# Kernel tuning notes

Hardware: AMD Instinct MI355X
Metric: run time of the kernel (lower is better)

Reference implementation:

```python
import jax, jax.numpy as jnp
import numpy as np
import math

N_COARSE, N_FINE = 8192, 32768
DEC_DIM, ENC_DIM, OUT_DIM, K = 256, 128, 128, 16
LN_EPS = 1e-5


def setup_inputs() -> dict:
    key = jax.random.key(0)
    ks = jax.random.split(key, 16)
    s = lambda fan_in: 1.0 / math.sqrt(fan_in)
    return {
        "decoder_features": jax.random.normal(ks[0], (N_COARSE, DEC_DIM), jnp.float32),
        "decoder_pos": jax.random.normal(ks[1], (N_COARSE, 3), jnp.float32),
        "encoder_features": jax.random.normal(ks[2], (N_FINE, ENC_DIM), jnp.float32),
        "encoder_pos": jax.random.normal(ks[3], (N_FINE, 3), jnp.float32),
        "encoder_labels": jax.random.randint(ks[4], (N_FINE,), 0, 13, jnp.int64),
        # params (torch nn.Linear default init scale)
        "Wq": jax.random.uniform(ks[5], (DEC_DIM, ENC_DIM), jnp.float32, -s(ENC_DIM), s(ENC_DIM)),
        "bq": jnp.zeros((DEC_DIM,), jnp.float32),
        "Wk": jax.random.uniform(ks[6], (DEC_DIM, DEC_DIM), jnp.float32, -s(DEC_DIM), s(DEC_DIM)),
        "bk": jnp.zeros((DEC_DIM,), jnp.float32),
        "Wv": jax.random.uniform(ks[7], (DEC_DIM, DEC_DIM), jnp.float32, -s(DEC_DIM), s(DEC_DIM)),
        "bv": jnp.zeros((DEC_DIM,), jnp.float32),
        "W1": jax.random.uniform(ks[8], (OUT_DIM, DEC_DIM + ENC_DIM), jnp.float32, -s(DEC_DIM + ENC_DIM), s(DEC_DIM + ENC_DIM)),
        "b1": jnp.zeros((OUT_DIM,), jnp.float32),
        "W2": jax.random.uniform(ks[9], (OUT_DIM, OUT_DIM), jnp.float32, -s(OUT_DIM), s(OUT_DIM)),
        "b2": jnp.zeros((OUT_DIM,), jnp.float32),
        "ln_g": jnp.ones((OUT_DIM,), jnp.float32),
        "ln_b": jnp.zeros((OUT_DIM,), jnp.float32),
    }


def _knn_indices(encoder_pos, decoder_pos, k):
    # For each fine (encoder) point, k nearest coarse (decoder) points.
    # squared distances [N_fine, N_coarse]
    d2 = (
        jnp.sum(encoder_pos * encoder_pos, axis=1, keepdims=True)
        - 2.0 * encoder_pos @ decoder_pos.T
        + jnp.sum(decoder_pos * decoder_pos, axis=1)[None, :]
    )
    _, idx = jax.lax.top_k(-d2, k)  # [N_fine, K]
    return idx


def reference(decoder_features, decoder_pos, encoder_features, encoder_pos,
              encoder_labels, Wq, bq, Wk, bk, Wv, bv, W1, b1, W2, b2, ln_g, ln_b):
    idx = _knn_indices(encoder_pos, decoder_pos, K)            # [Nf, K]
    nbr = decoder_features[idx]                                 # [Nf, K, Dd]
    query = encoder_features @ Wq.T + bq                        # [Nf, Dd]
    keys = nbr @ Wk.T + bk                                      # [Nf, K, Dd]
    values = nbr @ Wv.T + bv                                    # [Nf, K, Dd]
    scores = jnp.einsum('nd,nkd->nk', query, keys) / math.sqrt(DEC_DIM)
    # segment softmax over edges grouped by fine target == softmax over K
    weights = jax.nn.softmax(scores, axis=-1)                   # [Nf, K]
    agg = jnp.einsum('nk,nkd->nd', weights, values)             # [Nf, Dd]
    combined = jnp.concatenate([agg, encoder_features], axis=-1)
    h = jax.nn.relu(combined @ W1.T + b1)
    up = h @ W2.T + b2                                          # [Nf, out]
    mu = jnp.mean(up, axis=-1, keepdims=True)
    var = jnp.var(up, axis=-1, keepdims=True)
    out = (up - mu) * jax.lax.rsqrt(var + LN_EPS) * ln_g + ln_b
    # dropout is identity in eval mode
    return (out, encoder_pos, encoder_labels)
```

## Files before the change

kernel.cpp:

```cpp
#include <hip/hip_runtime.h>
#include <hip/hip_bf16.h>

typedef __hip_bfloat16 bf16;
typedef unsigned short u16;

#define NC 8192
#define NF 32768
#define DD 256
#define DE 128
#define KNN 16
#define FMAXV 3.402823466e+38f

__device__ __forceinline__ float bfbits2f(u16 u){
  union { unsigned u; float f; } x; x.u = ((unsigned)u) << 16; return x.f;
}

__global__ __launch_bounds__(256) void k_prep(const float* __restrict__ dpos,
                                              const float* __restrict__ Wk,
                                              const float* __restrict__ Wv,
                                              const float* __restrict__ W1,
                                              const float* __restrict__ W2,
                                              float4* __restrict__ pos4,
                                              float4* __restrict__ WkS,
                                              float4* __restrict__ WvS,
                                              float4* __restrict__ W1aS,
                                              float4* __restrict__ W1eSa,
                                              float4* __restrict__ W1eSb,
                                              float4* __restrict__ W2Sa,
                                              float4* __restrict__ W2Sb){
  int g = blockIdx.x * 256 + threadIdx.x;
  if (g < 8192){
    float x = dpos[g * 3 + 0], y = dpos[g * 3 + 1], z = dpos[g * 3 + 2];
    float dd = __fadd_rn(__fadd_rn(__fmul_rn(x,x), __fmul_rn(y,y)), __fmul_rn(z,z));
    pos4[g] = make_float4(x, y, z, dd * 0.5f);
  } else if (g < 24576){
    int f = g - 8192; int c4 = f >> 8, t = f & 255;
    WkS[f] = ((const float4*)(Wk + (size_t)t * 256))[c4];
  } else if (g < 40960){
    int f = g - 24576; int c4 = f >> 8, t = f & 255;
    WvS[f] = ((const float4*)(Wv + (size_t)t * 256))[c4];
  } else if (g < 49152){
    int f = g - 40960; int c4 = f >> 7, h = f & 127;
    W1aS[f] = ((const float4*)(W1 + (size_t)h * 384))[c4];
  } else if (g < 51200){
    int f = g - 49152; int c4 = f >> 6, jg = f & 63;
    W1eSa[f] = ((const float4*)(W1 + (size_t)(2 * jg) * 384 + 256))[c4];
  } else if (g < 53248){
    int f = g - 51200; int c4 = f >> 6, jg = f & 63;
    W1eSb[f] = ((const float4*)(W1 + (size_t)(2 * jg + 1) * 384 + 256))[c4];
  } else if (g < 55296){
    int f = g - 53248; int c4 = f >> 6, jg = f & 63;
    W2Sa[f] = ((const float4*)(W2 + (size_t)(2 * jg) * 128))[c4];
  } else if (g < 57344){
    int f = g - 55296; int c4 = f >> 6, jg = f & 63;
    W2Sb[f] = ((const float4*)(W2 + (size_t)(2 * jg + 1) * 128))[c4];
  }
}

__global__ __launch_bounds__(256) void k_dec(const float* __restrict__ df,
                                             const float* __restrict__ Wq, const float* __restrict__ bq,
                                             const float4* __restrict__ WkS, const float* __restrict__ bk,
                                             const float4* __restrict__ WvS, const float* __restrict__ bv,
                                             const float4* __restrict__ W1aS,
                                             bf16* __restrict__ Zd, bf16* __restrict__ Ud,
                                             float* __restrict__ bqK){
  __shared__ float bufA[16 * 256];
  __shared__ float bufB[16 * 256];
  int t = threadIdx.x;
  int g0 = blockIdx.x * 16;
  for (int r = 0; r < 16; ++r)
    bufA[r * 256 + t] = df[(size_t)(g0 + r) * 256 + t];
  __syncthreads();
  float accK[16], accV[16];
  #pragma unroll
  for (int p = 0; p < 16; ++p){ accK[p] = 0.f; accV[p] = 0.f; }
  const float4* A4 = (const float4*)bufA;
  for (int c4 = 0; c4 < 64; ++c4){
    float4 wk = WkS[c4 * 256 + t];
    float4 wv = WvS[c4 * 256 + t];
    #pragma unroll
    for (int p = 0; p < 16; ++p){
      float4 a = A4[p * 64 + c4];
      accK[p] += wk.x*a.x + wk.y*a.y + wk.z*a.z + wk.w*a.w;
      accV[p] += wv.x*a.x + wv.y*a.y + wv.z*a.z + wv.w*a.w;
    }
  }
  float bkj = bk[t];
  float bvj = bv[t];
  __syncthreads();
  #pragma unroll
  for (int p = 0; p < 16; ++p){
    bufA[p * 256 + t] = accK[p] + bkj;
    bufB[p * 256 + t] = accV[p] + bvj;
  }
  __syncthreads();
  if (t < 16){
    float s = 0.f;
    for (int j = 0; j < 256; ++j) s += bq[j] * bufA[t * 256 + j];
    bqK[g0 + t] = s;
  }
  {
    int c = t & 127, pg = t >> 7;
    float acc[8];
    #pragma unroll
    for (int pp = 0; pp < 8; ++pp) acc[pp] = 0.f;
    for (int j0 = 0; j0 < 256; j0 += 8){
      float w[8];
      #pragma unroll
      for (int jj = 0; jj < 8; ++jj)
        w[jj] = Wq[(size_t)(j0 + jj) * 128 + c];
      #pragma unroll
      for (int pp = 0; pp < 8; ++pp){
        float4 a = ((const float4*)bufA)[(pg * 8 + pp) * 64 + (j0 >> 2)];
        float4 b = ((const float4*)bufA)[(pg * 8 + pp) * 64 + (j0 >> 2) + 1];
        acc[pp] += w[0]*a.x + w[1]*a.y + w[2]*a.z + w[3]*a.w
                 + w[4]*b.x + w[5]*b.y + w[6]*b.z + w[7]*b.w;
      }
    }
    #pragma unroll
    for (int pp = 0; pp < 8; ++pp)
      Zd[(size_t)(g0 + pg * 8 + pp) * 128 + c] = __float2bfloat16(acc[pp]);
  }
  {
    int h = t & 127, pg = t >> 7;
    float acc[8];
    #pragma unroll
    for (int pp = 0; pp < 8; ++pp) acc[pp] = 0.f;
    for (int c4 = 0; c4 < 64; ++c4){
      float4 w = W1aS[c4 * 128 + h];
      #pragma unroll
      for (int pp = 0; pp < 8; ++pp){
        float4 a = ((const float4*)bufB)[(pg * 8 + pp) * 64 + c4];
        acc[pp] += w.x*a.x + w.y*a.y + w.z*a.z + w.w*a.w;
      }
    }
    #pragma unroll
    for (int pp = 0; pp < 8; ++pp)
      Ud[(size_t)(g0 + pg * 8 + pp) * 128 + h] = __float2bfloat16(acc[pp]);
  }
}

__global__ __launch_bounds__(256) void k_attn(const float* __restrict__ epos,
                                              const float4* __restrict__ pos4,
                                              const float* __restrict__ ef,
                                              const bf16* __restrict__ Zd,
                                              const bf16* __restrict__ Ud,
                                              const float* __restrict__ bqK,
                                              bf16* __restrict__ hagg){
  __shared__ float smin[4 * 64];
  __shared__ float tauLDS[4];
  __shared__ int   cnt[4];
  __shared__ float lval[4][64];
  __shared__ int   lidx[4][64];

  int t = threadIdx.x, lane = t & 63, w = t >> 6;
  int n0 = blockIdx.x * 4;
  float ex[4], ey[4], ez[4];
  #pragma unroll
  for (int p = 0; p < 4; ++p){
    ex[p] = epos[(n0 + p) * 3 + 0];
    ey[p] = epos[(n0 + p) * 3 + 1];
    ez[p] = epos[(n0 + p) * 3 + 2];
  }
  const float4* base = pos4 + w * 2048;

  float vmin[4] = {FMAXV, FMAXV, FMAXV, FMAXV};
  #pragma unroll 4
  for (int s = 0; s < 32; ++s){
    float4 P = base[s * 64 + lane];
    #pragma unroll
    for (int p = 0; p < 4; ++p){
      float ed = fmaf(ez[p], P.z, fmaf(ey[p], P.y, ex[p] * P.x));
      vmin[p] = fminf(vmin[p], P.w - ed);
    }
  }
  #pragma unroll
  for (int k = 2; k <= 64; k <<= 1){
    #pragma unroll
    for (int j = k >> 1; j > 0; j >>= 1){
      bool keepmin = ((lane & j) == 0) == ((lane & k) == 0);
      #pragma unroll
      for (int p = 0; p < 4; ++p){
        float pv = __shfl_xor(vmin[p], j);
        vmin[p] = keepmin ? fminf(vmin[p], pv) : fmaxf(vmin[p], pv);
      }
    }
  }
  if (lane < 16){
    #pragma unroll
    for (int p = 0; p < 4; ++p) smin[p * 64 + w * 16 + lane] = vmin[p];
  }
  if (t < 4) cnt[t] = 0;
  __syncthreads();
  {
    float v = smin[w * 64 + lane];
    #pragma unroll
    for (int k = 2; k <= 64; k <<= 1){
      #pragma unroll
      for (int j = k >> 1; j > 0; j >>= 1){
        float pv = __shfl_xor(v, j);
        bool keepmin = ((lane & j) == 0) == ((lane & k) == 0);
        v = keepmin ? fminf(v, pv) : fmaxf(v, pv);
      }
    }
    if (lane == 16) tauLDS[w] = v;
  }
  __syncthreads();
  float tau0[4];
  #pragma unroll
  for (int p = 0; p < 4; ++p) tau0[p] = tauLDS[p];

  #pragma unroll 2
  for (int s = 0; s < 32; ++s){
    float4 P = base[s * 64 + lane];
    int cand = w * 2048 + s * 64 + lane;
    #pragma unroll
    for (int p = 0; p < 4; ++p){
      float ed = fmaf(ez[p], P.z, fmaf(ey[p], P.y, ex[p] * P.x));
      float val = P.w - ed;
      if (val <= tau0[p]){
        int slot = atomicAdd(&cnt[p], 1);
        if (slot < 64){ lval[p][slot] = val; lidx[p][slot] = cand; }
      }
    }
  }
  __syncthreads();

  int n = n0 + w;
  int c = cnt[w]; if (c > 64) c = 64;
  float v  = (lane < c) ? lval[w][lane] : FMAXV;
  int   id = (lane < c) ? lidx[w][lane] : 0x7fffffff;
  #pragma unroll
  for (int k = 2; k <= 64; k <<= 1){
    #pragma unroll
    for (int j = k >> 1; j > 0; j >>= 1){
      float pv  = __shfl_xor(v, j);
      int   pid = __shfl_xor(id, j);
      bool keepmin = ((lane & j) == 0) == ((lane & k) == 0);
      bool pless = (pv < v) || (pv == v && pid < id);
      bool take = keepmin ? pless : !pless;
      if (take){ v = pv; id = pid; }
    }
  }
  int topi = id;

  float2 eu = *(const float2*)(ef + (size_t)n * 128 + lane * 2);
  float sc = -FMAXV;
  #pragma unroll
  for (int k = 0; k < KNN; ++k){
    int ik = __shfl(topi, k);
    ushort2 zu = *(const ushort2*)((const u16*)Zd + (size_t)ik * 128 + lane * 2);
    float p = eu.x * bfbits2f(zu.x) + eu.y * bfbits2f(zu.y);
    #pragma unroll
    for (int off = 32; off >= 1; off >>= 1) p += __shfl_xor(p, off);
    float bz = bqK[ik];
    if (lane == k) sc = (p + bz) * (1.0f / 16.0f);
  }
  float mx = sc;
  #pragma unroll
  for (int off = 8; off >= 1; off >>= 1) mx = fmaxf(mx, __shfl_xor(mx, off));
  float e = (lane < KNN) ? __expf(sc - mx) : 0.f;
  float l = e;
  #pragma unroll
  for (int off = 8; off >= 1; off >>= 1) l += __shfl_xor(l, off);
  float wgt = (lane < KNN) ? (e / l) : 0.f;

  float a0 = 0.f, a1 = 0.f;
  #pragma unroll
  for (int k = 0; k < KNN; ++k){
    int ik = __shfl(topi, k);
    float wk = __shfl(wgt, k);
    ushort2 uu = *(const ushort2*)((const u16*)Ud + (size_t)ik * 128 + lane * 2);
    a0 = fmaf(wk, bfbits2f(uu.x), a0);
    a1 = fmaf(wk, bfbits2f(uu.y), a1);
  }
  bf16* hr = hagg + (size_t)n * 128 + lane * 2;
  hr[0] = __float2bfloat16(a0);
  hr[1] = __float2bfloat16(a1);
}

__global__ __launch_bounds__(256) void k_mlp(const bf16* __restrict__ hagg, const float* __restrict__ ef,
                                             const float4* __restrict__ W1eSa, const float4* __restrict__ W1eSb,
                                             const float* __restrict__ b1,
                                             const float4* __restrict__ W2Sa, const float4* __restrict__ W2Sb,
                                             const float* __restrict__ b2,
                                             const float* __restrict__ lng, const float* __restrict__ lnb,
                                             const float* __restrict__ epos, const int* __restrict__ lab,
                                             float* __restrict__ out){
  __shared__ float efs[16 * 128];
  __shared__ float hgs[16 * 128];
  __shared__ float hbuf[16 * 128];
  __shared__ float ubuf[16 * 128];
  __shared__ float stats[32];
  int t = threadIdx.x;
  int n0 = blockIdx.x * 16;
  {
    int gid = blockIdx.x * 256 + t;
    if (gid < NF){
      float* op = out + (size_t)NF * 128;
      op[gid * 3 + 0] = epos[gid * 3 + 0];
      op[gid * 3 + 1] = epos[gid * 3 + 1];
      op[gid * 3 + 2] = epos[gid * 3 + 2];
      out[(size_t)NF * 128 + (size_t)NF * 3 + gid] = (float)lab[gid];
    }
  }
  for (int f = t; f < 2048; f += 256){
    int r = f >> 7, c = f & 127;
    efs[f] = ef[(size_t)(n0 + r) * 128 + c];
    hgs[f] = __bfloat162float(hagg[(size_t)(n0 + r) * 128 + c]);
  }
  __syncthreads();
  int jg = t & 63, pg = t >> 6;
  int j0 = jg * 2, p0 = pg * 4;
  float acc[2][4];
  #pragma unroll
  for (int a = 0; a < 2; ++a)
    #pragma unroll
    for (int p = 0; p < 4; ++p) acc[a][p] = 0.f;
  const float4* efs4 = (const float4*)efs;
  for (int c4 = 0; c4 < 32; ++c4){
    float4 wa = W1eSa[c4 * 64 + jg], wb = W1eSb[c4 * 64 + jg];
    #pragma unroll
    for (int p = 0; p < 4; ++p){
      float4 x = efs4[(p0 + p) * 32 + c4];
      acc[0][p] += wa.x*x.x + wa.y*x.y + wa.z*x.z + wa.w*x.w;
      acc[1][p] += wb.x*x.x + wb.y*x.y + wb.z*x.z + wb.w*x.w;
    }
  }
  float b1a = b1[j0], b1b = b1[j0 + 1];
  #pragma unroll
  for (int p = 0; p < 4; ++p){
    hbuf[(p0 + p) * 128 + j0]     = fmaxf(acc[0][p] + b1a + hgs[(p0 + p) * 128 + j0],     0.f);
    hbuf[(p0 + p) * 128 + j0 + 1] = fmaxf(acc[1][p] + b1b + hgs[(p0 + p) * 128 + j0 + 1], 0.f);
  }
  __syncthreads();
  float acc2[2][4];
  #pragma unroll
  for (int a = 0; a < 2; ++a)
    #pragma unroll
    for (int p = 0; p < 4; ++p) acc2[a][p] = 0.f;
  const float4* hb4 = (const float4*)hbuf;
  for (int c4 = 0; c4 < 32; ++c4){
    float4 wa = W2Sa[c4 * 64 + jg], wb = W2Sb[c4 * 64 + jg];
    #pragma unroll
    for (int p = 0; p < 4; ++p){
      float4 x = hb4[(p0 + p) * 32 + c4];
      acc2[0][p] += wa.x*x.x + wa.y*x.y + wa.z*x.z + wa.w*x.w;
      acc2[1][p] += wb.x*x.x + wb.y*x.y + wb.z*x.z + wb.w*x.w;
    }
  }
  float b2a = b2[j0], b2b = b2[j0 + 1];
  float u[2][4];
  #pragma unroll
  for (int p = 0; p < 4; ++p){
    u[0][p] = acc2[0][p] + b2a;
    u[1][p] = acc2[1][p] + b2b;
    ubuf[(p0 + p) * 128 + j0]     = u[0][p];
    ubuf[(p0 + p) * 128 + j0 + 1] = u[1][p];
  }
  __syncthreads();
  {
    int p = t >> 4, qi = t & 15;
    const float* ub = &ubuf[p * 128 + qi * 8];
    float s = 0.f, s2 = 0.f;
    #pragma unroll
    for (int e2i = 0; e2i < 8; ++e2i){ float v = ub[e2i]; s += v; s2 += v * v; }
    #pragma unroll
    for (int off = 1; off < 16; off <<= 1){ s += __shfl_xor(s, off); s2 += __shfl_xor(s2, off); }
    if (qi == 0){
      float mu = s * (1.f / 128.f);
      float var = s2 * (1.f / 128.f) - mu * mu;
      stats[p] = mu;
      stats[16 + p] = rsqrtf(fmaxf(var, 0.f) + 1e-5f);
    }
  }
  __syncthreads();
  float ga = lng[j0], gb = lng[j0 + 1];
  float ba = lnb[j0], bbv = lnb[j0 + 1];
  #pragma unroll
  for (int p = 0; p < 4; ++p){
    float mu = stats[p0 + p], rs = stats[16 + p0 + p];
    out[(size_t)(n0 + p0 + p) * 128 + j0]     = (u[0][p] - mu) * rs * ga + ba;
    out[(size_t)(n0 + p0 + p) * 128 + j0 + 1] = (u[1][p] - mu) * rs * gb + bbv;
  }
}

extern "C" void kernel_launch(void* const* d_in, const int* in_sizes, int n_in,
                              void* d_out, int out_size, void* d_ws, size_t ws_size,
                              hipStream_t stream){
  const float* df   = (const float*)d_in[0];
  const float* dpos = (const float*)d_in[1];
  const float* ef   = (const float*)d_in[2];
  const float* epos = (const float*)d_in[3];
  const int*   lab  = (const int*)d_in[4];
  const float* Wq = (const float*)d_in[5];
  const float* bq = (const float*)d_in[6];
  const float* Wk = (const float*)d_in[7];
  const float* bk = (const float*)d_in[8];
  const float* Wv = (const float*)d_in[9];
  const float* bv = (const float*)d_in[10];
  const float* W1 = (const float*)d_in[11];
  const float* b1 = (const float*)d_in[12];
  const float* W2 = (const float*)d_in[13];
  const float* b2 = (const float*)d_in[14];
  const float* lng = (const float*)d_in[15];
  const float* lnb = (const float*)d_in[16];
  float* out = (float*)d_out;

  char* wsb = (char*)d_ws;
  float4* pos4  = (float4*)(wsb);
  bf16*   Zd    = (bf16*)(wsb + 131072);
  bf16*   Ud    = (bf16*)(wsb + 2228224);
  float*  bqK   = (float*)(wsb + 4325376);
  bf16*   hagg  = (bf16*)(wsb + 4358144);
  float4* WkS   = (float4*)(wsb + 12746752);
  float4* WvS   = (float4*)(wsb + 13008896);
  float4* W1aS  = (float4*)(wsb + 13271040);
  float4* W1eSa = (float4*)(wsb + 13402112);
  float4* W1eSb = (float4*)(wsb + 13434880);
  float4* W2Sa  = (float4*)(wsb + 13467648);
  float4* W2Sb  = (float4*)(wsb + 13500416);

  k_prep <<<224, 256, 0, stream>>>(dpos, Wk, Wv, W1, W2, pos4, WkS, WvS, W1aS, W1eSa, W1eSb, W2Sa, W2Sb);
  k_dec  <<<NC / 16, 256, 0, stream>>>(df, Wq, bq, WkS, bk, WvS, bv, W1aS, Zd, Ud, bqK);
  k_attn <<<NF / 4, 256, 0, stream>>>(epos, pos4, ef, Zd, Ud, bqK, hagg);
  k_mlp  <<<NF / 16, 256, 0, stream>>>(hagg, ef, W1eSa, W1eSb, b1, W2Sa, W2Sb, b2, lng, lnb, epos, lab, out);
  (void)in_sizes; (void)n_in; (void)out_size; (void)ws_size;
}
```

Before: 374.0 us.

## Split decoder and MLP kernels to drop shared-memory staging and raise occupancy

Splits the decoder projection kernel into two launches (K/V projection to global memory, then Q- and W1-folding projections), and splits the MLP kernel into a first-layer kernel and a second-layer-plus-LayerNorm kernel. Operands are now read directly from global memory (uniform per wave) instead of being staged in LDS, which removes large shared buffers and barriers and should let more blocks run concurrently. Wq is pre-transposed into a float4 layout in the prep kernel, and the kNN distance is folded into a single FMA chain. The cost is two extra launches and fp32 round-trips of K/V and the hidden activations through global memory.

```diff
diff --git a/kernel.cpp b/kernel.cpp
--- a/kernel.cpp
+++ b/kernel.cpp
@@ -6,8 +6,6 @@
 
 #define NC 8192
 #define NF 32768
-#define DD 256
-#define DE 128
 #define KNN 16
 #define FMAXV 3.402823466e+38f
 
@@ -20,10 +18,12 @@
                                               const float* __restrict__ Wv,
                                               const float* __restrict__ W1,
                                               const float* __restrict__ W2,
+                                              const float* __restrict__ Wq,
                                               float4* __restrict__ pos4,
                                               float4* __restrict__ WkS,
                                               float4* __restrict__ WvS,
                                               float4* __restrict__ W1aS,
+                                              float4* __restrict__ WqS,
                                               float4* __restrict__ W1eSa,
                                               float4* __restrict__ W1eSb,
                                               float4* __restrict__ W2Sa,
@@ -54,89 +54,74 @@
   } else if (g < 57344){
     int f = g - 55296; int c4 = f >> 6, jg = f & 63;
     W2Sb[f] = ((const float4*)(W2 + (size_t)(2 * jg + 1) * 128))[c4];
-  }
-}
-
-__global__ __launch_bounds__(256) void k_dec(const float* __restrict__ df,
-                                             const float* __restrict__ Wq, const float* __restrict__ bq,
-                                             const float4* __restrict__ WkS, const float* __restrict__ bk,
-                                             const float4* __restrict__ WvS, const float* __restrict__ bv,
-                                             const float4* __restrict__ W1aS,
-                                             bf16* __restrict__ Zd, bf16* __restrict__ Ud,
-                                             float* __restrict__ bqK){
-  __shared__ float bufA[16 * 256];
-  __shared__ float bufB[16 * 256];
+  } else if (g < 65536){
+    int f = g - 57344; int j4 = f >> 7, c = f & 127;
+    WqS[f] = make_float4(Wq[(size_t)(j4 * 4 + 0) * 128 + c],
+                         Wq[(size_t)(j4 * 4 + 1) * 128 + c],
+                         Wq[(size_t)(j4 * 4 + 2) * 128 + c],
+                         Wq[(size_t)(j4 * 4 + 3) * 128 + c]);
+  }
+}
+
+__global__ __launch_bounds__(256) void k_dec1(const float* __restrict__ df,
+                                              const float4* __restrict__ WkS, const float* __restrict__ bk,
+                                              const float4* __restrict__ WvS, const float* __restrict__ bv,
+                                              float* __restrict__ Kg, float* __restrict__ Vg){
   int t = threadIdx.x;
   int g0 = blockIdx.x * 16;
-  for (int r = 0; r < 16; ++r)
-    bufA[r * 256 + t] = df[(size_t)(g0 + r) * 256 + t];
-  __syncthreads();
   float accK[16], accV[16];
   #pragma unroll
   for (int p = 0; p < 16; ++p){ accK[p] = 0.f; accV[p] = 0.f; }
-  const float4* A4 = (const float4*)bufA;
   for (int c4 = 0; c4 < 64; ++c4){
     float4 wk = WkS[c4 * 256 + t];
     float4 wv = WvS[c4 * 256 + t];
     #pragma unroll
     for (int p = 0; p < 16; ++p){
-      float4 a = A4[p * 64 + c4];
+      float4 a = ((const float4*)(df + (size_t)(g0 + p) * 256))[c4];
       accK[p] += wk.x*a.x + wk.y*a.y + wk.z*a.z + wk.w*a.w;
       accV[p] += wv.x*a.x + wv.y*a.y + wv.z*a.z + wv.w*a.w;
     }
   }
-  float bkj = bk[t];
-  float bvj = bv[t];
-  __syncthreads();
+  float bkj = bk[t], bvj = bv[t];
   #pragma unroll
   for (int p = 0; p < 16; ++p){
-    bufA[p * 256 + t] = accK[p] + bkj;
-    bufB[p * 256 + t] = accV[p] + bvj;
-  }
-  __syncthreads();
+    Kg[(size_t)(g0 + p) * 256 + t] = accK[p] + bkj;
+    Vg[(size_t)(g0 + p) * 256 + t] = accV[p] + bvj;
+  }
+}
+
+__global__ __launch_bounds__(256) void k_dec2(const float* __restrict__ Kg,
+                                              const float* __restrict__ Vg,
+                                              const float4* __restrict__ WqS,
+                                              const float4* __restrict__ W1aS,
+                                              const float* __restrict__ bq,
+                                              bf16* __restrict__ Zd, bf16* __restrict__ Ud,
+                                              float* __restrict__ bqK){
+  int t = threadIdx.x;
+  int g0 = blockIdx.x * 16;
+  int half = __builtin_amdgcn_readfirstlane(t >> 7);
+  int c = t & 127;
+  const float*  src = half ? Vg : Kg;
+  const float4* W   = half ? W1aS : WqS;
+  float acc[16];
+  #pragma unroll
+  for (int p = 0; p < 16; ++p) acc[p] = 0.f;
+  for (int j4 = 0; j4 < 64; ++j4){
+    float4 w = W[j4 * 128 + c];
+    #pragma unroll
+    for (int p = 0; p < 16; ++p){
+      float4 a = ((const float4*)(src + (size_t)(g0 + p) * 256))[j4];
+      acc[p] += w.x*a.x + w.y*a.y + w.z*a.z + w.w*a.w;
+    }
+  }
+  bf16* dst = half ? Ud : Zd;
+  #pragma unroll
+  for (int p = 0; p < 16; ++p)
+    dst[(size_t)(g0 + p) * 128 + c] = __float2bfloat16(acc[p]);
   if (t < 16){
     float s = 0.f;
-    for (int j = 0; j < 256; ++j) s += bq[j] * bufA[t * 256 + j];
+    for (int j = 0; j < 256; ++j) s += bq[j] * Kg[(size_t)(g0 + t) * 256 + j];
     bqK[g0 + t] = s;
-  }
-  {
-    int c = t & 127, pg = t >> 7;
-    float acc[8];
-    #pragma unroll
-    for (int pp = 0; pp < 8; ++pp) acc[pp] = 0.f;
-    for (int j0 = 0; j0 < 256; j0 += 8){
-      float w[8];
-      #pragma unroll
-      for (int jj = 0; jj < 8; ++jj)
-        w[jj] = Wq[(size_t)(j0 + jj) * 128 + c];
-      #pragma unroll
-      for (int pp = 0; pp < 8; ++pp){
-        float4 a = ((const float4*)bufA)[(pg * 8 + pp) * 64 + (j0 >> 2)];
-        float4 b = ((const float4*)bufA)[(pg * 8 + pp) * 64 + (j0 >> 2) + 1];
-        acc[pp] += w[0]*a.x + w[1]*a.y + w[2]*a.z + w[3]*a.w
-                 + w[4]*b.x + w[5]*b.y + w[6]*b.z + w[7]*b.w;
-      }
-    }
-    #pragma unroll
-    for (int pp = 0; pp < 8; ++pp)
-      Zd[(size_t)(g0 + pg * 8 + pp) * 128 + c] = __float2bfloat16(acc[pp]);
-  }
-  {
-    int h = t & 127, pg = t >> 7;
-    float acc[8];
-    #pragma unroll
-    for (int pp = 0; pp < 8; ++pp) acc[pp] = 0.f;
-    for (int c4 = 0; c4 < 64; ++c4){
-      float4 w = W1aS[c4 * 128 + h];
-      #pragma unroll
-      for (int pp = 0; pp < 8; ++pp){
-        float4 a = ((const float4*)bufB)[(pg * 8 + pp) * 64 + c4];
-        acc[pp] += w.x*a.x + w.y*a.y + w.z*a.z + w.w*a.w;
-      }
-    }
-    #pragma unroll
-    for (int pp = 0; pp < 8; ++pp)
-      Ud[(size_t)(g0 + pg * 8 + pp) * 128 + h] = __float2bfloat16(acc[pp]);
   }
 }
 
@@ -155,12 +140,12 @@
 
   int t = threadIdx.x, lane = t & 63, w = t >> 6;
   int n0 = blockIdx.x * 4;
-  float ex[4], ey[4], ez[4];
+  float nex[4], ney[4], nez[4];
   #pragma unroll
   for (int p = 0; p < 4; ++p){
-    ex[p] = epos[(n0 + p) * 3 + 0];
-    ey[p] = epos[(n0 + p) * 3 + 1];
-    ez[p] = epos[(n0 + p) * 3 + 2];
+    nex[p] = -epos[(n0 + p) * 3 + 0];
+    ney[p] = -epos[(n0 + p) * 3 + 1];
+    nez[p] = -epos[(n0 + p) * 3 + 2];
   }
   const float4* base = pos4 + w * 2048;
 
@@ -170,8 +155,8 @@
     float4 P = base[s * 64 + lane];
     #pragma unroll
     for (int p = 0; p < 4; ++p){
-      float ed = fmaf(ez[p], P.z, fmaf(ey[p], P.y, ex[p] * P.x));
-      vmin[p] = fminf(vmin[p], P.w - ed);
+      float val = fmaf(nez[p], P.z, fmaf(ney[p], P.y, fmaf(nex[p], P.x, P.w)));
+      vmin[p] = fminf(vmin[p], val);
     }
   }
   #pragma unroll
@@ -216,8 +201,7 @@
     int cand = w * 2048 + s * 64 + lane;
     #pragma unroll
     for (int p = 0; p < 4; ++p){
-      float ed = fmaf(ez[p], P.z, fmaf(ey[p], P.y, ex[p] * P.x));
-      float val = P.w - ed;
+      float val = fmaf(nez[p], P.z, fmaf(ney[p], P.y, fmaf(nex[p], P.x, P.w)));
       if (val <= tau0[p]){
         int slot = atomicAdd(&cnt[p], 1);
         if (slot < 64){ lval[p][slot] = val; lidx[p][slot] = cand; }
@@ -279,17 +263,50 @@
   hr[1] = __float2bfloat16(a1);
 }
 
-__global__ __launch_bounds__(256) void k_mlp(const bf16* __restrict__ hagg, const float* __restrict__ ef,
-                                             const float4* __restrict__ W1eSa, const float4* __restrict__ W1eSb,
-                                             const float* __restrict__ b1,
-                                             const float4* __restrict__ W2Sa, const float4* __restrict__ W2Sb,
-                                             const float* __restrict__ b2,
-                                             const float* __restrict__ lng, const float* __restrict__ lnb,
-                                             const float* __restrict__ epos, const int* __restrict__ lab,
-                                             float* __restrict__ out){
-  __shared__ float efs[16 * 128];
-  __shared__ float hgs[16 * 128];
-  __shared__ float hbuf[16 * 128];
+__global__ __launch_bounds__(256) void k_mlp1(const bf16* __restrict__ hagg,
+                                              const float* __restrict__ ef,
+                                              const float4* __restrict__ W1eSa,
+                                              const float4* __restrict__ W1eSb,
+                                              const float* __restrict__ b1,
+                                              float* __restrict__ hg){
+  int t = threadIdx.x;
+  int jg = t & 63;
+  int pg4 = __builtin_amdgcn_readfirstlane((t >> 6) * 4);
+  int n0 = blockIdx.x * 16;
+  int j0 = jg * 2;
+  float acc[2][4];
+  #pragma unroll
+  for (int a = 0; a < 2; ++a)
+    #pragma unroll
+    for (int p = 0; p < 4; ++p) acc[a][p] = 0.f;
+  for (int c4 = 0; c4 < 32; ++c4){
+    float4 wa = W1eSa[c4 * 64 + jg];
+    float4 wb = W1eSb[c4 * 64 + jg];
+    #pragma unroll
+    for (int p = 0; p < 4; ++p){
+      float4 x = ((const float4*)(ef + (size_t)(n0 + pg4 + p) * 128))[c4];
+      acc[0][p] += wa.x*x.x + wa.y*x.y + wa.z*x.z + wa.w*x.w;
+      acc[1][p] += wb.x*x.x + wb.y*x.y + wb.z*x.z + wb.w*x.w;
+    }
+  }
+  float b1a = b1[j0], b1b = b1[j0 + 1];
+  #pragma unroll
+  for (int p = 0; p < 4; ++p){
+    size_t row = (size_t)(n0 + pg4 + p);
+    ushort2 hgv = *(const ushort2*)((const u16*)hagg + row * 128 + j0);
+    float h0 = fmaxf(acc[0][p] + b1a + bfbits2f(hgv.x), 0.f);
+    float h1 = fmaxf(acc[1][p] + b1b + bfbits2f(hgv.y), 0.f);
+    *(float2*)(hg + row * 128 + j0) = make_float2(h0, h1);
+  }
+}
+
+__global__ __launch_bounds__(256) void k_mlp2(const float* __restrict__ hg,
+                                              const float4* __restrict__ W2Sa,
+                                              const float4* __restrict__ W2Sb,
+                                              const float* __restrict__ b2,
+                                              const float* __restrict__ lng, const float* __restrict__ lnb,
+                                              const float* __restrict__ epos, const int* __restrict__ lab,
+                                              float* __restrict__ out){
   __shared__ float ubuf[16 * 128];
   __shared__ float stats[32];
   int t = threadIdx.x;
@@ -304,47 +321,20 @@
       out[(size_t)NF * 128 + (size_t)NF * 3 + gid] = (float)lab[gid];
     }
   }
-  for (int f = t; f < 2048; f += 256){
-    int r = f >> 7, c = f & 127;
-    efs[f] = ef[(size_t)(n0 + r) * 128 + c];
-    hgs[f] = __bfloat162float(hagg[(size_t)(n0 + r) * 128 + c]);
-  }
-  __syncthreads();
-  int jg = t & 63, pg = t >> 6;
-  int j0 = jg * 2, p0 = pg * 4;
-  float acc[2][4];
+  int jg = t & 63;
+  int pg4 = __builtin_amdgcn_readfirstlane((t >> 6) * 4);
+  int j0 = jg * 2;
+  float acc2[2][4];
   #pragma unroll
   for (int a = 0; a < 2; ++a)
     #pragma unroll
-    for (int p = 0; p < 4; ++p) acc[a][p] = 0.f;
-  const float4* efs4 = (const float4*)efs;
+    for (int p = 0; p < 4; ++p) acc2[a][p] = 0.f;
   for (int c4 = 0; c4 < 32; ++c4){
-    float4 wa = W1eSa[c4 * 64 + jg], wb = W1eSb[c4 * 64 + jg];
+    float4 wa = W2Sa[c4 * 64 + jg];
+    float4 wb = W2Sb[c4 * 64 + jg];
     #pragma unroll
     for (int p = 0; p < 4; ++p){
-      float4 x = efs4[(p0 + p) * 32 + c4];
-      acc[0][p] += wa.x*x.x + wa.y*x.y + wa.z*x.z + wa.w*x.w;
-      acc[1][p] += wb.x*x.x + wb.y*x.y + wb.z*x.z + wb.w*x.w;
-    }
-  }
-  float b1a = b1[j0], b1b = b1[j0 + 1];
-  #pragma unroll
-  for (int p = 0; p < 4; ++p){
-    hbuf[(p0 + p) * 128 + j0]     = fmaxf(acc[0][p] + b1a + hgs[(p0 + p) * 128 + j0],     0.f);
-    hbuf[(p0 + p) * 128 + j0 + 1] = fmaxf(acc[1][p] + b1b + hgs[(p0 + p) * 128 + j0 + 1], 0.f);
-  }
-  __syncthreads();
-  float acc2[2][4];
-  #pragma unroll
-  for (int a = 0; a < 2; ++a)
-    #pragma unroll
-    for (int p = 0; p < 4; ++p) acc2[a][p] = 0.f;
-  const float4* hb4 = (const float4*)hbuf;
-  for (int c4 = 0; c4 < 32; ++c4){
-    float4 wa = W2Sa[c4 * 64 + jg], wb = W2Sb[c4 * 64 + jg];
-    #pragma unroll
-    for (int p = 0; p < 4; ++p){
-      float4 x = hb4[(p0 + p) * 32 + c4];
+      float4 x = ((const float4*)(hg + (size_t)(n0 + pg4 + p) * 128))[c4];
       acc2[0][p] += wa.x*x.x + wa.y*x.y + wa.z*x.z + wa.w*x.w;
       acc2[1][p] += wb.x*x.x + wb.y*x.y + wb.z*x.z + wb.w*x.w;
     }
@@ -355,8 +345,8 @@
   for (int p = 0; p < 4; ++p){
     u[0][p] = acc2[0][p] + b2a;
     u[1][p] = acc2[1][p] + b2b;
-    ubuf[(p0 + p) * 128 + j0]     = u[0][p];
-    ubuf[(p0 + p) * 128 + j0 + 1] = u[1][p];
+    ubuf[(pg4 + p) * 128 + j0]     = u[0][p];
+    ubuf[(pg4 + p) * 128 + j0 + 1] = u[1][p];
   }
   __syncthreads();
   {
@@ -379,9 +369,9 @@
   float ba = lnb[j0], bbv = lnb[j0 + 1];
   #pragma unroll
   for (int p = 0; p < 4; ++p){
-    float mu = stats[p0 + p], rs = stats[16 + p0 + p];
-    out[(size_t)(n0 + p0 + p) * 128 + j0]     = (u[0][p] - mu) * rs * ga + ba;
-    out[(size_t)(n0 + p0 + p) * 128 + j0 + 1] = (u[1][p] - mu) * rs * gb + bbv;
+    float mu = stats[pg4 + p], rs = stats[16 + pg4 + p];
+    out[(size_t)(n0 + pg4 + p) * 128 + j0]     = (u[0][p] - mu) * rs * ga + ba;
+    out[(size_t)(n0 + pg4 + p) * 128 + j0 + 1] = (u[1][p] - mu) * rs * gb + bbv;
   }
 }
 
@@ -416,14 +406,20 @@
   float4* WkS   = (float4*)(wsb + 12746752);
   float4* WvS   = (float4*)(wsb + 13008896);
   float4* W1aS  = (float4*)(wsb + 13271040);
-  float4* W1eSa = (float4*)(wsb + 13402112);
-  float4* W1eSb = (float4*)(wsb + 13434880);
-  float4* W2Sa  = (float4*)(wsb + 13467648);
-  float4* W2Sb  = (float4*)(wsb + 13500416);
-
-  k_prep <<<224, 256, 0, stream>>>(dpos, Wk, Wv, W1, W2, pos4, WkS, WvS, W1aS, W1eSa, W1eSb, W2Sa, W2Sb);
-  k_dec  <<<NC / 16, 256, 0, stream>>>(df, Wq, bq, WkS, bk, WvS, bv, W1aS, Zd, Ud, bqK);
+  float4* WqS   = (float4*)(wsb + 13402112);
+  float4* W1eSa = (float4*)(wsb + 13533184);
+  float4* W1eSb = (float4*)(wsb + 13565952);
+  float4* W2Sa  = (float4*)(wsb + 13598720);
+  float4* W2Sb  = (float4*)(wsb + 13631488);
+  float*  Kg    = (float*)(wsb + 13664256);
+  float*  Vg    = (float*)(wsb + 22052864);
+  float*  hg    = (float*)(wsb + 13664256);
+
+  k_prep <<<256, 256, 0, stream>>>(dpos, Wk, Wv, W1, W2, Wq, pos4, WkS, WvS, W1aS, WqS, W1eSa, W1eSb, W2Sa, W2Sb);
+  k_dec1 <<<NC / 16, 256, 0, stream>>>(df, WkS, bk, WvS, bv, Kg, Vg);
+  k_dec2 <<<NC / 16, 256, 0, stream>>>(Kg, Vg, WqS, W1aS, bq, Zd, Ud, bqK);
   k_attn <<<NF / 4, 256, 0, stream>>>(epos, pos4, ef, Zd, Ud, bqK, hagg);
-  k_mlp  <<<NF / 16, 256, 0, stream>>>(hagg, ef, W1eSa, W1eSb, b1, W2Sa, W2Sb, b2, lng, lnb, epos, lab, out);
+  k_mlp1 <<<NF / 16, 256, 0, stream>>>(hagg, ef, W1eSa, W1eSb, b1, hg);
+  k_mlp2 <<<NF / 16, 256, 0, stream>>>(hg, W2Sa, W2Sb, b2, lng, lnb, epos, lab, out);
   (void)in_sizes; (void)n_in; (void)out_size; (void)ws_size;
 }
```

Result: slower. 399.9 us (+6.9%).
